# Performance work log

Hardware: AMD Instinct MI355X
Metric: run time of the kernel (lower is better)

The kernel has to match this reference:

```python
import jax, jax.numpy as jnp
import numpy as np

BOUND = np.array([[-4.0, 4.0], [-4.0, 4.0], [-2.0, 2.0]], dtype=np.float32)
N_PTS = 1048576
PLANE_C = 3
PLANE_RES = [128, 256, 512, 1024]
N_LEVELS = 16
F_PER = 2
T = 2 ** 16  # hashmap size (log2_hashmap_size=16)
BASE_RES = 16
FINEST = int(float((BOUND[:, 1] - BOUND[:, 0]).max()) / 0.02)  # 400
_growth = np.exp(np.log(FINEST / BASE_RES) / (N_LEVELS - 1))
HASH_RES = np.floor(BASE_RES * _growth ** np.arange(N_LEVELS)).astype(np.float32)
PRIMES = jnp.array([1, 2654435761, 805459861], dtype=jnp.uint32)


def setup_inputs() -> dict:
    key = jax.random.key(0)
    ks = jax.random.split(key, 32)
    lo = jnp.asarray(BOUND[:, 0]); hi = jnp.asarray(BOUND[:, 1])
    inp = {}
    inp['p'] = jax.random.uniform(ks[0], (N_PTS, 3), dtype=jnp.float32) * (hi - lo) + lo
    i = 1
    for li, r in enumerate(PLANE_RES):
        for name in ('xy', 'xz', 'yz'):
            inp[f'plane_{name}_{li}'] = 0.1 * jax.random.normal(ks[i], (PLANE_C, r, r), dtype=jnp.float32)
            i += 1
    inp['hash_table'] = jax.random.uniform(ks[i], (N_LEVELS, T, F_PER), dtype=jnp.float32, minval=-1e-4, maxval=1e-4); i += 1

    def lin(k, fi, fo):
        s = 1.0 / np.sqrt(fi)
        k1, k2 = jax.random.split(k)
        return (jax.random.uniform(k1, (fi, fo), minval=-s, maxval=s, dtype=jnp.float32),
                jax.random.uniform(k2, (fo,), minval=-s, maxval=s, dtype=jnp.float32))

    c_in = 12 * PLANE_C + N_LEVELS * F_PER  # 68
    inp['W0'], inp['b0'] = lin(ks[i], c_in, 64); i += 1
    inp['W1'], inp['b1'] = lin(ks[i], 64, 64); i += 1
    inp['Wo'], inp['bo'] = lin(ks[i], 64, 33); i += 1  # 1 sdf + 32 geo_feat
    inp['Wc0'], inp['bc0'] = lin(ks[i], 12 * PLANE_C + 32, 64); i += 1
    inp['Wc1'], inp['bc1'] = lin(ks[i], 64, 32); i += 1
    inp['Wco'], inp['bco'] = lin(ks[i], 32, 3); i += 1
    return inp


def sample_plane(plane, u, v):
    """Bilinear grid_sample, align_corners=True, padding_mode='border'.
    plane: (C,H,W); u indexes W, v indexes H; u,v in [-1,1]. Returns (N,C)."""
    C, H, W = plane.shape
    x = jnp.clip((u + 1.0) * 0.5 * (W - 1), 0.0, W - 1)
    y = jnp.clip((v + 1.0) * 0.5 * (H - 1), 0.0, H - 1)
    x0 = jnp.floor(x); y0 = jnp.floor(y)
    wx = x - x0; wy = y - y0
    x0i = x0.astype(jnp.int32); y0i = y0.astype(jnp.int32)
    x1i = jnp.minimum(x0i + 1, W - 1); y1i = jnp.minimum(y0i + 1, H - 1)
    g = lambda yi, xi: plane[:, yi, xi]  # (C,N)
    out = (g(y0i, x0i) * ((1 - wy) * (1 - wx)) + g(y0i, x1i) * ((1 - wy) * wx)
           + g(y1i, x0i) * (wy * (1 - wx)) + g(y1i, x1i) * (wy * wx))
    return out.T


def hash_encode(p01, table):
    """Multi-res hash grid (instant-ngp style). p01: (N,3) in [0,1]; table: (L,T,F) -> (N, L*F)."""
    res = jnp.asarray(HASH_RES)  # (L,)

    def level(r, tab):
        x = p01 * r
        x0 = jnp.floor(x)
        w = x - x0
        xi = x0.astype(jnp.uint32)  # (N,3)
        feat = jnp.zeros((p01.shape[0], F_PER), dtype=table.dtype)
        for dz in (0, 1):
            for dy in (0, 1):
                for dx in (0, 1):
                    c = xi + jnp.array([dx, dy, dz], dtype=jnp.uint32)
                    h = c * PRIMES[None, :]
                    idx = ((h[:, 0] ^ h[:, 1] ^ h[:, 2]) % T).astype(jnp.int32)
                    wgt = ((w[:, 0] if dx else 1 - w[:, 0])
                           * (w[:, 1] if dy else 1 - w[:, 1])
                           * (w[:, 2] if dz else 1 - w[:, 2]))
                    feat = feat + tab[idx] * wgt[:, None]
        return feat  # (N,F)

    feats = jax.vmap(level, in_axes=(0, 0))(res, table)  # (L,N,F)
    return jnp.transpose(feats, (1, 0, 2)).reshape(p01.shape[0], N_LEVELS * F_PER)


def _forward(p, plane_xy_0, plane_xz_0, plane_yz_0, plane_xy_1, plane_xz_1, plane_yz_1,
             plane_xy_2, plane_xz_2, plane_yz_2, plane_xy_3, plane_xz_3, plane_yz_3,
             hash_table, W0, b0, W1, b1, Wo, bo, Wc0, bc0, Wc1, bc1, Wco, bco):
    bound = jnp.asarray(BOUND)
    p_nor = (p - bound[:, 0]) / (bound[:, 1] - bound[:, 0]) * 2.0 - 1.0  # normalize_3d_coordinate
    u, v, w = p_nor[:, 0], p_nor[:, 1], p_nor[:, 2]
    levels = [(plane_xy_0, plane_xz_0, plane_yz_0), (plane_xy_1, plane_xz_1, plane_yz_1),
              (plane_xy_2, plane_xz_2, plane_yz_2), (plane_xy_3, plane_xz_3, plane_yz_3)]
    feats = []
    for pxy, pxz, pyz in levels:
        feats += [sample_plane(pxy, u, v), sample_plane(pxz, u, w), sample_plane(pyz, v, w)]
    plane_feat = jnp.concatenate(feats, axis=-1)  # (N, 36)
    hfeat = hash_encode((p_nor + 1.0) * 0.5, hash_table)  # (N, 32)
    # SDF branch
    h = jnp.concatenate([plane_feat, hfeat], axis=-1)  # (N, 68)
    h = jax.nn.relu(h @ W0 + b0)
    h = jax.nn.relu(h @ W1 + b1)
    sf = jnp.tanh(h @ Wo + bo)
    sdf, geo_feat = sf[:, :1], sf[:, 1:]
    # RGB branch
    c = jnp.concatenate([geo_feat, plane_feat], axis=-1)  # (N, 68)
    c = jax.nn.relu(c @ Wc0 + bc0)
    c = jax.nn.relu(c @ Wc1 + bc1)
    rgb = jax.nn.sigmoid(c @ Wco + bco)
    return jnp.concatenate([rgb, sdf], axis=-1)  # (N, 4)


def reference(p, plane_xy_0, plane_xz_0, plane_yz_0, plane_xy_1, plane_xz_1, plane_yz_1,
              plane_xy_2, plane_xz_2, plane_yz_2, plane_xy_3, plane_xz_3, plane_yz_3,
              hash_table, W0, b0, W1, b1, Wo, bo, Wc0, bc0, Wc1, bc1, Wco, bco):
    return _forward(p, plane_xy_0, plane_xz_0, plane_yz_0, plane_xy_1, plane_xz_1, plane_yz_1,
                    plane_xy_2, plane_xz_2, plane_yz_2, plane_xy_3, plane_xz_3, plane_yz_3,
                    hash_table, W0, b0, W1, b1, Wo, bo, Wc0, bc0, Wc1, bc1, Wco, bco)
```

## Files before the change

### kernel.cpp

```cpp
#include <hip/hip_runtime.h>

#define NPTS 1048576
#define NBKT 262144

typedef short bhalf8 __attribute__((ext_vector_type(8)));
typedef _Float16 halfv8 __attribute__((ext_vector_type(8)));
typedef float floatx4 __attribute__((ext_vector_type(4)));

#define WSZ 24320
#define FROWS 21
#define MLP_THREADS 1024
#define MLP_WAVES 16

#define PB_PLANES 16320
#define PB_HASH 4096
#define PB_HIST 4096

__device__ const float HRg[16] = {16.f, 19.f, 24.f, 30.f, 37.f, 46.f, 57.f, 71.f,
                                  89.f, 110.f, 136.f, 169.f, 210.f, 260.f, 322.f, 400.f};


__device__ __forceinline__ float my_tanh(float x) {
  float e = __expf(2.f * x);
  return 1.f - 2.f * __builtin_amdgcn_rcpf(e + 1.f);
}

__device__ __forceinline__ float my_sigmoid(float x) {
  return __builtin_amdgcn_rcpf(1.f + __expf(-x));
}

__device__ __forceinline__ unsigned short f2h(float v) {
  _Float16 h = (_Float16)v;
  unsigned short u;
  __builtin_memcpy(&u, &h, 2);
  return u;
}

__device__ __forceinline__ float h2f(unsigned short u) {
  _Float16 h;
  __builtin_memcpy(&h, &u, 2);
  return (float)h;
}

__device__ __forceinline__ float texch(uint2 t, int c) {
  unsigned short u = (c == 0) ? (unsigned short)(t.x & 0xffffu)
                   : (c == 1) ? (unsigned short)(t.x >> 16)
                              : (unsigned short)(t.y & 0xffffu);
  return h2f(u);
}

__device__ __forceinline__ unsigned mort6(unsigned x) {
  return (x & 1) | ((x & 2) << 2) | ((x & 4) << 4) |
         ((x & 8) << 6) | ((x & 16) << 8) | ((x & 32) << 10);
}

__device__ __forceinline__ unsigned morton_key(float px, float py, float pz) {
  float qx = (px + 4.f) * 0.125f, qy = (py + 4.f) * 0.125f, qz = (pz + 2.f) * 0.25f;
  unsigned kx = min(63, max(0, (int)(qx * 64.f)));
  unsigned ky = min(63, max(0, (int)(qy * 64.f)));
  unsigned kz = min(63, max(0, (int)(qz * 64.f)));
  return mort6(kx) | (mort6(ky) << 1) | (mort6(kz) << 2);
}

__device__ __forceinline__ unsigned hash_level(const unsigned* __restrict__ ht, int lv,
                                               float q0, float q1, float q2) {
  const float r = HRg[lv];
  float x0 = q0 * r, x1 = q1 * r, x2 = q2 * r;
  float f0 = floorf(x0), f1 = floorf(x1), f2 = floorf(x2);
  float w0 = x0 - f0, w1 = x1 - f1, w2 = x2 - f2;
  unsigned i0 = (unsigned)(int)f0, i1 = (unsigned)(int)f1, i2 = (unsigned)(int)f2;
  const unsigned* __restrict__ hb = ht + ((unsigned)lv << 16);
  unsigned tv[8];
#pragma unroll
  for (int dz = 0; dz < 2; ++dz)
#pragma unroll
    for (int dy = 0; dy < 2; ++dy)
#pragma unroll
      for (int dx = 0; dx < 2; ++dx) {
        unsigned h = (i0 + dx) ^ ((i1 + dy) * 2654435761u) ^ ((i2 + dz) * 805459861u);
        tv[dz * 4 + dy * 2 + dx] = hb[h & 65535u];
      }
  float a0 = 0.f, a1 = 0.f;
#pragma unroll
  for (int c = 0; c < 8; ++c) {
    const int dx = c & 1, dy = (c >> 1) & 1, dz = c >> 2;
    float wgt = (dx ? w0 : 1.f - w0) * (dy ? w1 : 1.f - w1) * (dz ? w2 : 1.f - w2);
    a0 = fmaf(h2f((unsigned short)(tv[c] & 0xffffu)), wgt, a0);
    a1 = fmaf(h2f((unsigned short)(tv[c] >> 16)), wgt, a1);
  }
  return (unsigned)f2h(a0) | ((unsigned)f2h(a1) << 16);
}


struct PrepParams {
  const float* psrc[12];
  ushort4* pdst[12];
  const float* hash;
  unsigned* hashb;
  const float* p;
  unsigned* hist;
};

__global__ __launch_bounds__(256) void prep_kernel(PrepParams P) {
  const int b = blockIdx.x;
  if (b < PB_PLANES) {
    const int CUM[13] = {0, 16384, 32768, 49152, 114688, 180224, 245760,
                         507904, 770048, 1032192, 2080768, 3129344, 4177920};
    const int RESL[12] = {128, 128, 128, 256, 256, 256, 512, 512, 512, 1024, 1024, 1024};
    const int s = b << 8;
    int pi = 0;
#pragma unroll
    for (int i = 1; i < 12; ++i)
      if (s >= CUM[i]) pi = i;
    const int li = s + threadIdx.x - CUM[pi];
    const int R = RESL[pi];
    const int n = R * R;
    const float* __restrict__ src = P.psrc[pi];
    ushort4 t;
    t.x = f2h(src[li]);
    t.y = f2h(src[n + li]);
    t.z = f2h(src[2 * n + li]);
    t.w = 0;
    P.pdst[pi][li] = t;
  } else if (b < PB_PLANES + PB_HASH) {
    const int i = ((b - PB_PLANES) << 8) + threadIdx.x;
    float2 v = *(const float2*)(P.hash + (size_t)i * 2);
    P.hashb[i] = (unsigned)f2h(v.x) | ((unsigned)f2h(v.y) << 16);
  } else {
    const int i = ((b - PB_PLANES - PB_HASH) << 8) + threadIdx.x;
    const float* pp = P.p + (size_t)i * 3;
    unsigned k = morton_key(pp[0], pp[1], pp[2]);
    atomicAdd(&P.hist[k], 1u);
  }
}


__global__ __launch_bounds__(256) void scan1_kernel(const unsigned* __restrict__ hist,
                                                    unsigned* __restrict__ partial) {
  __shared__ unsigned s[256];
  const int b = blockIdx.x, t = threadIdx.x;
  uint4 v = ((const uint4*)(hist + b * 1024))[t];
  s[t] = v.x + v.y + v.z + v.w;
  __syncthreads();
  for (int d = 128; d > 0; d >>= 1) {
    if (t < d) s[t] += s[t + d];
    __syncthreads();
  }
  if (t == 0) partial[b] = s[0];
}

__global__ __launch_bounds__(256) void scan2_kernel(const unsigned* __restrict__ partial,
                                                    unsigned* __restrict__ base) {
  __shared__ unsigned s[256];
  const int t = threadIdx.x;
  s[t] = partial[t];
  __syncthreads();
  for (int d = 1; d < 256; d <<= 1) {
    unsigned v = (t >= d) ? s[t - d] : 0u;
    __syncthreads();
    s[t] += v;
    __syncthreads();
  }
  base[t] = (t == 0) ? 0u : s[t - 1];
}

__global__ __launch_bounds__(256) void scan3_kernel(const unsigned* __restrict__ hist,
                                                    const unsigned* __restrict__ base,
                                                    unsigned* __restrict__ cursor) {
  __shared__ unsigned s[256];
  const int b = blockIdx.x, t = threadIdx.x;
  uint4 v = ((const uint4*)(hist + b * 1024))[t];
  unsigned sum = v.x + v.y + v.z + v.w;
  s[t] = sum;
  __syncthreads();
  for (int d = 1; d < 256; d <<= 1) {
    unsigned x = (t >= d) ? s[t - d] : 0u;
    __syncthreads();
    s[t] += x;
    __syncthreads();
  }
  unsigned off = base[b] + s[t] - sum;
  uint4 c;
  c.x = off;
  c.y = off + v.x;
  c.z = off + v.x + v.y;
  c.w = off + v.x + v.y + v.z;
  ((uint4*)(cursor + b * 1024))[t] = c;
}

__global__ __launch_bounds__(256) void scatter_kernel(const float* __restrict__ p,
                                                      unsigned* __restrict__ cursor,
                                                      unsigned* __restrict__ perm) {
  int i = blockIdx.x * 256 + threadIdx.x;
  const float* pp = p + (size_t)i * 3;
  unsigned k = morton_key(pp[0], pp[1], pp[2]);
  unsigned slot = atomicAdd(&cursor[k], 1u);
  perm[slot] = (unsigned)i;
}


__global__ __launch_bounds__(256) void repack_plane(const float* __restrict__ src,
                                                    ushort4* __restrict__ dst, int R) {
  int i = blockIdx.x * 256 + threadIdx.x;
  int n = R * R;
  if (i >= n) return;
  ushort4 t;
  t.x = f2h(src[i]);
  t.y = f2h(src[n + i]);
  t.z = f2h(src[2 * n + i]);
  t.w = 0;
  dst[i] = t;
}


__device__ __forceinline__ void sample3i(const uint2* __restrict__ pl,
                                         float a, float b, int R, float* f) {
  const float Rm1 = (float)(R - 1);
  float x = fminf(fmaxf((a + 1.f) * 0.5f * Rm1, 0.f), Rm1);
  float y = fminf(fmaxf((b + 1.f) * 0.5f * Rm1, 0.f), Rm1);
  float x0f = floorf(x), y0f = floorf(y);
  float wx = x - x0f, wy = y - y0f;
  int x0 = (int)x0f, y0 = (int)y0f;
  int x1 = min(x0 + 1, R - 1), y1 = min(y0 + 1, R - 1);
  float w00 = (1.f - wy) * (1.f - wx);
  float w01 = (1.f - wy) * wx;
  float w10 = wy * (1.f - wx);
  float w11 = wy * wx;
  uint2 t00 = pl[y0 * R + x0];
  uint2 t01 = pl[y0 * R + x1];
  uint2 t10 = pl[y1 * R + x0];
  uint2 t11 = pl[y1 * R + x1];
#pragma unroll
  for (int c = 0; c < 3; ++c) {
    f[c] = texch(t00, c) * w00 + texch(t01, c) * w01 +
           texch(t10, c) * w10 + texch(t11, c) * w11;
  }
}

__device__ __forceinline__ void sample3f(const float* __restrict__ pl,
                                         float a, float b, int R, float* f) {
  const float Rm1 = (float)(R - 1);
  float x = fminf(fmaxf((a + 1.f) * 0.5f * Rm1, 0.f), Rm1);
  float y = fminf(fmaxf((b + 1.f) * 0.5f * Rm1, 0.f), Rm1);
  float x0f = floorf(x), y0f = floorf(y);
  float wx = x - x0f, wy = y - y0f;
  int x0 = (int)x0f, y0 = (int)y0f;
  int x1 = min(x0 + 1, R - 1), y1 = min(y0 + 1, R - 1);
  float w00 = (1.f - wy) * (1.f - wx);
  float w01 = (1.f - wy) * wx;
  float w10 = wy * (1.f - wx);
  float w11 = wy * wx;
  int i00 = y0 * R + x0, i01 = y0 * R + x1;
  int i10 = y1 * R + x0, i11 = y1 * R + x1;
  const int R2 = R * R;
#pragma unroll
  for (int c = 0; c < 3; ++c) {
    const float* base = pl + c * R2;
    f[c] = base[i00] * w00 + base[i01] * w01 + base[i10] * w10 + base[i11] * w11;
  }
}


struct FeatParams {
  const float* p;
  const uint2* pli[12];
  const unsigned* perm;
  unsigned* fbuf;
};

template <bool SORT>
__global__ __launch_bounds__(256) void feat_kernel(FeatParams P) {
  int bid = blockIdx.x;
  if (SORT) bid = (bid & 7) * (NPTS / 256 / 8) + (bid >> 3);
  const int tid = bid * 256 + threadIdx.x;
  const int pid = SORT ? (int)P.perm[tid] : tid;

  const float* __restrict__ pp = P.p + (size_t)pid * 3;
  const float px = pp[0], py = pp[1], pz = pp[2];

  const float u = (px + 4.f) * 0.25f - 1.f;
  const float v = (py + 4.f) * 0.25f - 1.f;
  const float w = (pz + 2.f) * 0.5f - 1.f;

  float pf[36];
  {
    const int RES[4] = {128, 256, 512, 1024};
#pragma unroll
    for (int li = 0; li < 4; ++li) {
      sample3i(P.pli[li * 3 + 0], u, v, RES[li], &pf[li * 9 + 0]);
      sample3i(P.pli[li * 3 + 1], u, w, RES[li], &pf[li * 9 + 3]);
      sample3i(P.pli[li * 3 + 2], v, w, RES[li], &pf[li * 9 + 6]);
    }
  }
  unsigned* __restrict__ F = P.fbuf;
#pragma unroll
  for (int kk = 0; kk < 18; ++kk) {
    unsigned pk = (unsigned)f2h(pf[2 * kk]) | ((unsigned)f2h(pf[2 * kk + 1]) << 16);
    F[(size_t)kk * NPTS + tid] = pk;
  }
  F[(size_t)18 * NPTS + tid] = __float_as_uint((px + 4.f) * 0.125f);
  F[(size_t)19 * NPTS + tid] = __float_as_uint((py + 4.f) * 0.125f);
  F[(size_t)20 * NPTS + tid] = __float_as_uint((pz + 2.f) * 0.25f);
}


struct MlpWParams {
  const unsigned* fbuf;
  const unsigned* perm;
  const unsigned* hashb;
  const float* W0; const float* b0;
  const float* W1; const float* b1;
  const float* Wo; const float* bo;
  const float* Wc0; const float* bc0;
  const float* Wc1; const float* bc1;
  const float* Wco; const float* bco;
  float* out;
};

__device__ __forceinline__ void stage_w(const float* __restrict__ src, int K, int Nsrc,
                                        int STR, int NPAD, int OFF, short* Wlds, int tid) {
  const int total = NPAD * STR;
  for (int idx = tid; idx < total; idx += MLP_THREADS) {
    int c = idx / STR;
    int k = idx - c * STR;
    float val = (k < K && c < Nsrc) ? src[k * Nsrc + c] : 0.f;
    Wlds[OFF + idx] = (short)f2h(val);
  }
}

__device__ __forceinline__ void stage_b(const float* __restrict__ src, int Nsrc, int NPAD,
                                        int BOFF, float* Blds, int tid) {
  for (int j = tid; j < NPAD; j += MLP_THREADS) Blds[BOFF + j] = (j < Nsrc) ? src[j] : 0.f;
}

__device__ __forceinline__ halfv8 as_h8(bhalf8 s) {
  halfv8 h;
  __builtin_memcpy(&h, &s, 16);
  return h;
}

__device__ __forceinline__ halfv8 ldA(const unsigned* __restrict__ fbuf, int pt,
                                      int kkBase, int kkLim) {
  bhalf8 r;
#pragma unroll
  for (int j = 0; j < 4; ++j) {
    const int kk = kkBase + j;
    unsigned d = 0u;
    if (kk < kkLim) d = fbuf[(size_t)kk * NPTS + pt];
    r[2 * j] = (short)(d & 0xffffu);
    r[2 * j + 1] = (short)(d >> 16);
  }
  return as_h8(r);
}

__device__ __forceinline__ halfv8 frag4(unsigned d0, unsigned d1, unsigned d2, unsigned d3) {
  bhalf8 r;
  r[0] = (short)(d0 & 0xffffu); r[1] = (short)(d0 >> 16);
  r[2] = (short)(d1 & 0xffffu); r[3] = (short)(d1 >> 16);
  r[4] = (short)(d2 & 0xffffu); r[5] = (short)(d2 >> 16);
  r[6] = (short)(d3 & 0xffffu); r[7] = (short)(d3 >> 16);
  return as_h8(r);
}

__device__ __forceinline__ halfv8 ldS(const short* scr, int rowl, int grp, int s) {
  return *(const halfv8*)&scr[rowl * 72 + 32 * s + 8 * grp];
}

template <int NT, int KS, int OFF, int STR>
__device__ __forceinline__ void mlayer(const halfv8 (&af)[KS], floatx4 (&acc)[NT],
                                       const short* Wlds, int rowl, int grp) {
#pragma unroll
  for (int n = 0; n < NT; ++n) {
    floatx4 a{};
#pragma unroll
    for (int s = 0; s < KS; ++s) {
      const int wo = OFF + (16 * n + rowl) * STR + 32 * s + 8 * grp;
      const halfv8 bh = *(const halfv8*)&Wlds[wo];
      a = __builtin_amdgcn_mfma_f32_16x16x32_f16(af[s], bh, a, 0, 0, 0);
    }
    acc[n] = a;
  }
}

template <int NT>
__device__ __forceinline__ void relu_wr(const floatx4 (&acc)[NT], const float* Blds,
                                        int boff, short* scr, int rowl, int grp) {
#pragma unroll
  for (int n = 0; n < NT; ++n) {
    const float b = Blds[boff + 16 * n + rowl];
#pragma unroll
    for (int r = 0; r < 4; ++r) {
      float v = fmaxf(acc[n][r] + b, 0.f);
      scr[(grp * 4 + r) * 72 + 16 * n + rowl] = (short)f2h(v);
    }
  }
}

__device__ __forceinline__ void tanh_wr(const floatx4 (&acc)[3], const float* Blds,
                                        short* scr, float* ost, int rowl, int grp) {
#pragma unroll
  for (int n = 0; n < 3; ++n) {
    const float b = Blds[128 + 16 * n + rowl];
    const int c = 16 * n + rowl;
#pragma unroll
    for (int r = 0; r < 4; ++r) {
      float v = my_tanh(acc[n][r] + b);
      if (n == 0 && rowl == 0) ost[(grp * 4 + r) * 4 + 3] = v;
      if (c >= 1 && c <= 32) scr[(grp * 4 + r) * 72 + c - 1] = (short)f2h(v);
    }
  }
}

template <bool SORT>
__global__ __launch_bounds__(MLP_THREADS) void mlp_mfma(MlpWParams P) {
  __shared__ short Wlds[WSZ];
  __shared__ float Blds[288];
  __shared__ short Scr[MLP_WAVES * 16 * 72];
  __shared__ float Ost[MLP_WAVES][16][4];

  const int tid = threadIdx.x;

  stage_w(P.W0,  68, 64, 104, 64,     0, Wlds, tid);
  stage_w(P.W1,  64, 64,  72, 64,  6656, Wlds, tid);
  stage_w(P.Wo,  64, 33,  72, 48, 11264, Wlds, tid);
  stage_w(P.Wc0, 68, 64, 104, 64, 14720, Wlds, tid);
  stage_w(P.Wc1, 64, 32,  72, 32, 21376, Wlds, tid);
  stage_w(P.Wco, 32,  3,  40, 16, 23680, Wlds, tid);
  stage_b(P.b0,  64, 64,   0, Blds, tid);
  stage_b(P.b1,  64, 64,  64, Blds, tid);
  stage_b(P.bo,  33, 48, 128, Blds, tid);
  stage_b(P.bc0, 64, 64, 176, Blds, tid);
  stage_b(P.bc1, 32, 32, 240, Blds, tid);
  stage_b(P.bco,  3, 16, 272, Blds, tid);
  __syncthreads();

  const int wave = tid >> 6, lane = tid & 63;
  const int rowl = lane & 15, grp = lane >> 4;
  short* scr0 = &Scr[wave * 16 * 72];
  float* ost0 = &Ost[wave][0][0];

  const int lv0 = (grp == 0) ? 0 : (4 * grp - 2);

  for (int t = 0; t < 8; ++t) {
    const int wbase = ((blockIdx.x * 8 + t) * MLP_WAVES + wave) * 16;
    const int ptA = wbase + rowl;

    {
      const unsigned* __restrict__ F = P.fbuf;
      float qA0 = __uint_as_float(F[(size_t)18 * NPTS + ptA]);
      float qA1 = __uint_as_float(F[(size_t)19 * NPTS + ptA]);
      float qA2 = __uint_as_float(F[(size_t)20 * NPTS + ptA]);

      unsigned hA0, hA1, hA2, hA3;
      {
        const int l0 = lv0, l1 = lv0 + 1;
        const int l2 = (grp == 0) ? 14 : (lv0 + 2);
        const int l3 = (grp == 0) ? 15 : (lv0 + 3);
        hA0 = hash_level(P.hashb, l0, qA0, qA1, qA2);
        hA1 = hash_level(P.hashb, l1, qA0, qA1, qA2);
        hA2 = hash_level(P.hashb, l2, qA0, qA1, qA2);
        hA3 = hash_level(P.hashb, l3, qA0, qA1, qA2);
      }

      unsigned pA16 = F[(size_t)16 * NPTS + ptA], pA17 = F[(size_t)17 * NPTS + ptA];

      halfv8 s1A = (grp == 0) ? frag4(pA16, pA17, hA0, hA1) : frag4(hA0, hA1, hA2, hA3);
      halfv8 s2A = (grp == 0) ? frag4(hA2, hA3, 0u, 0u) : frag4(0u, 0u, 0u, 0u);

      halfv8 afA[3] = {ldA(P.fbuf, ptA, 4 * grp, 18), s1A, s2A};
      floatx4 accA[4];
      mlayer<4, 3, 0, 104>(afA, accA, Wlds, rowl, grp);
      relu_wr<4>(accA, Blds, 0, scr0, rowl, grp);
    }
    {
      halfv8 afA[2] = {ldS(scr0, rowl, grp, 0), ldS(scr0, rowl, grp, 1)};
      floatx4 accA[4];
      mlayer<4, 2, 6656, 72>(afA, accA, Wlds, rowl, grp);
      relu_wr<4>(accA, Blds, 64, scr0, rowl, grp);
    }
    {
      halfv8 afA[2] = {ldS(scr0, rowl, grp, 0), ldS(scr0, rowl, grp, 1)};
      floatx4 accA[3];
      mlayer<3, 2, 11264, 72>(afA, accA, Wlds, rowl, grp);
      tanh_wr(accA, Blds, scr0, ost0, rowl, grp);
    }
    {
      halfv8 afA[3] = {ldS(scr0, rowl, grp, 0),
                       ldA(P.fbuf, ptA, 0 + 4 * grp, 18),
                       ldA(P.fbuf, ptA, 16 + 4 * grp, 18)};
      floatx4 accA[4];
      mlayer<4, 3, 14720, 104>(afA, accA, Wlds, rowl, grp);
      relu_wr<4>(accA, Blds, 176, scr0, rowl, grp);
    }
    {
      halfv8 afA[2] = {ldS(scr0, rowl, grp, 0), ldS(scr0, rowl, grp, 1)};
      floatx4 accA[2];
      mlayer<2, 2, 21376, 72>(afA, accA, Wlds, rowl, grp);
      relu_wr<2>(accA, Blds, 240, scr0, rowl, grp);
    }
    {
      halfv8 afA[1] = {ldS(scr0, rowl, grp, 0)};
      floatx4 accA[1];
      mlayer<1, 1, 23680, 40>(afA, accA, Wlds, rowl, grp);
      const float b = Blds[272 + rowl];
#pragma unroll
      for (int r = 0; r < 4; ++r) {
        float vA = my_sigmoid(accA[0][r] + b);
        if (rowl < 3) ost0[(grp * 4 + r) * 4 + rowl] = vA;
      }
    }

    if (lane < 16) {
      float4 o = *(float4*)&Ost[wave][lane][0];
      int dst = SORT ? (int)P.perm[wbase + lane] : (wbase + lane);
      ((float4*)P.out)[dst] = o;
    }
  }
}


struct DecParams {
  const float* p;
  const float* pl[12];
  const uint2* pli[12];
  const float* hash;
  const float* W0; const float* b0;
  const float* W1; const float* b1;
  const float* Wo; const float* bo;
  const float* Wc0; const float* bc0;
  const float* Wc1; const float* bc1;
  const float* Wco; const float* bco;
  float* out;
};

template <bool ILV>
__global__ __launch_bounds__(256) void dec_kernel(DecParams P) {
  const int tid = blockIdx.x * 256 + threadIdx.x;

  const float* __restrict__ pp = P.p + (size_t)tid * 3;
  const float px = pp[0], py = pp[1], pz = pp[2];

  const float u = (px + 4.f) * 0.25f - 1.f;
  const float v = (py + 4.f) * 0.25f - 1.f;
  const float w = (pz + 2.f) * 0.5f - 1.f;

  float feat[68];
  {
    const int RES[4] = {128, 256, 512, 1024};
#pragma unroll
    for (int li = 0; li < 4; ++li) {
      if (ILV) {
        sample3i(P.pli[li * 3 + 0], u, v, RES[li], &feat[li * 9 + 0]);
        sample3i(P.pli[li * 3 + 1], u, w, RES[li], &feat[li * 9 + 3]);
        sample3i(P.pli[li * 3 + 2], v, w, RES[li], &feat[li * 9 + 6]);
      } else {
        sample3f(P.pl[li * 3 + 0], u, v, RES[li], &feat[li * 9 + 0]);
        sample3f(P.pl[li * 3 + 1], u, w, RES[li], &feat[li * 9 + 3]);
        sample3f(P.pl[li * 3 + 2], v, w, RES[li], &feat[li * 9 + 6]);
      }
    }
  }

  {
    const float q0 = (px + 4.f) * 0.125f;
    const float q1 = (py + 4.f) * 0.125f;
    const float q2 = (pz + 2.f) * 0.25f;
    const float* __restrict__ ht = P.hash;
#pragma unroll
    for (int l = 0; l < 16; ++l) {
      const float r = HRg[l];
      float x0 = q0 * r, x1 = q1 * r, x2 = q2 * r;
      float f0 = floorf(x0), f1 = floorf(x1), f2 = floorf(x2);
      float w0 = x0 - f0, w1 = x1 - f1, w2 = x2 - f2;
      unsigned i0 = (unsigned)(int)f0, i1 = (unsigned)(int)f1, i2 = (unsigned)(int)f2;
      float a0 = 0.f, a1 = 0.f;
#pragma unroll
      for (int dz = 0; dz < 2; ++dz)
#pragma unroll
        for (int dy = 0; dy < 2; ++dy)
#pragma unroll
          for (int dx = 0; dx < 2; ++dx) {
            unsigned h = (i0 + dx) ^ ((i1 + dy) * 2654435761u) ^ ((i2 + dz) * 805459861u);
            unsigned idx = h & 65535u;
            const float2 tv = *(const float2*)(ht + (((unsigned)l << 16) + idx) * 2);
            float wgt = (dx ? w0 : 1.f - w0) * (dy ? w1 : 1.f - w1) * (dz ? w2 : 1.f - w2);
            a0 = fmaf(tv.x, wgt, a0);
            a1 = fmaf(tv.y, wgt, a1);
          }
      feat[36 + l * 2] = a0;
      feat[36 + l * 2 + 1] = a1;
    }
  }

  float acc[64];
#pragma unroll
  for (int j = 0; j < 64; ++j) acc[j] = P.b0[j];
#pragma unroll
  for (int i = 0; i < 68; ++i) {
    const float a = feat[i];
    const float* wr = P.W0 + i * 64;
#pragma unroll
    for (int j = 0; j < 64; ++j) acc[j] = fmaf(a, wr[j], acc[j]);
  }
  float hid[64];
#pragma unroll
  for (int j = 0; j < 64; ++j) hid[j] = fmaxf(acc[j], 0.f);

#pragma unroll
  for (int j = 0; j < 64; ++j) acc[j] = P.b1[j];
#pragma unroll
  for (int i = 0; i < 64; ++i) {
    const float a = hid[i];
    const float* wr = P.W1 + i * 64;
#pragma unroll
    for (int j = 0; j < 64; ++j) acc[j] = fmaf(a, wr[j], acc[j]);
  }
#pragma unroll
  for (int j = 0; j < 64; ++j) hid[j] = fmaxf(acc[j], 0.f);

  float so[33];
#pragma unroll
  for (int j = 0; j < 33; ++j) so[j] = P.bo[j];
#pragma unroll
  for (int i = 0; i < 64; ++i) {
    const float a = hid[i];
    const float* wr = P.Wo + i * 33;
#pragma unroll
    for (int j = 0; j < 33; ++j) so[j] = fmaf(a, wr[j], so[j]);
  }
  const float sdf = my_tanh(so[0]);
  float geo[32];
#pragma unroll
  for (int j = 0; j < 32; ++j) geo[j] = my_tanh(so[j + 1]);

#pragma unroll
  for (int j = 0; j < 64; ++j) acc[j] = P.bc0[j];
#pragma unroll
  for (int i = 0; i < 32; ++i) {
    const float a = geo[i];
    const float* wr = P.Wc0 + i * 64;
#pragma unroll
    for (int j = 0; j < 64; ++j) acc[j] = fmaf(a, wr[j], acc[j]);
  }
#pragma unroll
  for (int i = 0; i < 36; ++i) {
    const float a = feat[i];
    const float* wr = P.Wc0 + (32 + i) * 64;
#pragma unroll
    for (int j = 0; j < 64; ++j) acc[j] = fmaf(a, wr[j], acc[j]);
  }
#pragma unroll
  for (int j = 0; j < 64; ++j) hid[j] = fmaxf(acc[j], 0.f);

  float c1[32];
#pragma unroll
  for (int j = 0; j < 32; ++j) c1[j] = P.bc1[j];
#pragma unroll
  for (int i = 0; i < 64; ++i) {
    const float a = hid[i];
    const float* wr = P.Wc1 + i * 32;
#pragma unroll
    for (int j = 0; j < 32; ++j) c1[j] = fmaf(a, wr[j], c1[j]);
  }

  float r0 = P.bco[0], r1 = P.bco[1], r2 = P.bco[2];
#pragma unroll
  for (int i = 0; i < 32; ++i) {
    const float a = fmaxf(c1[i], 0.f);
    r0 = fmaf(a, P.Wco[i * 3 + 0], r0);
    r1 = fmaf(a, P.Wco[i * 3 + 1], r1);
    r2 = fmaf(a, P.Wco[i * 3 + 2], r2);
  }

  float4 o;
  o.x = my_sigmoid(r0);
  o.y = my_sigmoid(r1);
  o.z = my_sigmoid(r2);
  o.w = sdf;
  ((float4*)P.out)[tid] = o;
}


extern "C" void kernel_launch(void* const* d_in, const int* in_sizes, int n_in,
                              void* d_out, int out_size, void* d_ws, size_t ws_size,
                              hipStream_t stream) {
  const int RES[4] = {128, 256, 512, 1024};
  const size_t planes_bytes = (size_t)3 * (128 * 128 + 256 * 256 + 512 * 512 + 1024 * 1024) * 8;
  const size_t hash_bytes = (size_t)16 * 65536 * 4;
  const size_t feat_bytes = (size_t)FROWS * NPTS * 4;
  const size_t perm_bytes = (size_t)NPTS * 4;
  const size_t hist_bytes = (size_t)NBKT * 4;
  const size_t need_full = planes_bytes + hash_bytes + feat_bytes + 64;
  const size_t need_sort = need_full + perm_bytes + 2 * hist_bytes + 4096;
  const size_t need_mid = planes_bytes + 64;

  char* wsp = (char*)d_ws;
  const float* p = (const float*)d_in[0];

  if (ws_size >= need_sort) {
    size_t off = 0;
    PrepParams PP;
    PP.p = p;
    PP.hash = (const float*)d_in[13];
    const uint2* pli[12];
    for (int i = 0; i < 12; ++i) {
      int R = RES[i / 3];
      PP.psrc[i] = (const float*)d_in[1 + i];
      PP.pdst[i] = (ushort4*)(wsp + off);
      pli[i] = (const uint2*)(wsp + off);
      off += (size_t)R * R * 8;
    }
    unsigned* hashb = (unsigned*)(wsp + off);
    PP.hashb = hashb;
    off += hash_bytes;
    unsigned* fbuf = (unsigned*)(wsp + off);
    off += feat_bytes;
    unsigned* perm = (unsigned*)(wsp + off);
    off += perm_bytes;
    unsigned* hist = (unsigned*)(wsp + off);
    off += hist_bytes;
    unsigned* cursor = (unsigned*)(wsp + off);
    off += hist_bytes;
    unsigned* partial = (unsigned*)(wsp + off);
    off += 1024;
    unsigned* base = (unsigned*)(wsp + off);
    off += 1024;
    PP.hist = hist;

    hipMemsetAsync(hist, 0, hist_bytes, stream);
    prep_kernel<<<PB_PLANES + PB_HASH + PB_HIST, 256, 0, stream>>>(PP);
    scan1_kernel<<<256, 256, 0, stream>>>(hist, partial);
    scan2_kernel<<<1, 256, 0, stream>>>(partial, base);
    scan3_kernel<<<256, 256, 0, stream>>>(hist, base, cursor);
    scatter_kernel<<<NPTS / 256, 256, 0, stream>>>(p, cursor, perm);

    FeatParams FP;
    FP.p = p;
    for (int i = 0; i < 12; ++i) FP.pli[i] = pli[i];
    FP.perm = perm;
    FP.fbuf = fbuf;
    feat_kernel<true><<<NPTS / 256, 256, 0, stream>>>(FP);

    MlpWParams MP;
    MP.fbuf = fbuf;
    MP.perm = perm;
    MP.hashb = hashb;
    MP.W0 = (const float*)d_in[14]; MP.b0 = (const float*)d_in[15];
    MP.W1 = (const float*)d_in[16]; MP.b1 = (const float*)d_in[17];
    MP.Wo = (const float*)d_in[18]; MP.bo = (const float*)d_in[19];
    MP.Wc0 = (const float*)d_in[20]; MP.bc0 = (const float*)d_in[21];
    MP.Wc1 = (const float*)d_in[22]; MP.bc1 = (const float*)d_in[23];
    MP.Wco = (const float*)d_in[24]; MP.bco = (const float*)d_in[25];
    MP.out = (float*)d_out;
    mlp_mfma<true><<<512, MLP_THREADS, 0, stream>>>(MP);
    return;
  }

  if (ws_size >= need_full) {
    size_t off = 0;
    PrepParams PP;
    PP.p = p;
    PP.hash = (const float*)d_in[13];
    const uint2* pli[12];
    for (int i = 0; i < 12; ++i) {
      int R = RES[i / 3];
      PP.psrc[i] = (const float*)d_in[1 + i];
      PP.pdst[i] = (ushort4*)(wsp + off);
      pli[i] = (const uint2*)(wsp + off);
      off += (size_t)R * R * 8;
    }
    unsigned* hashb = (unsigned*)(wsp + off);
    PP.hashb = hashb;
    off += hash_bytes;
    unsigned* fbuf = (unsigned*)(wsp + off);
    PP.hist = nullptr;

    prep_kernel<<<PB_PLANES + PB_HASH, 256, 0, stream>>>(PP);

    FeatParams FP;
    FP.p = p;
    for (int i = 0; i < 12; ++i) FP.pli[i] = pli[i];
    FP.perm = nullptr;
    FP.fbuf = fbuf;
    feat_kernel<false><<<NPTS / 256, 256, 0, stream>>>(FP);

    MlpWParams MP;
    MP.fbuf = fbuf;
    MP.perm = nullptr;
    MP.hashb = hashb;
    MP.W0 = (const float*)d_in[14]; MP.b0 = (const float*)d_in[15];
    MP.W1 = (const float*)d_in[16]; MP.b1 = (const float*)d_in[17];
    MP.Wo = (const float*)d_in[18]; MP.bo = (const float*)d_in[19];
    MP.Wc0 = (const float*)d_in[20]; MP.bc0 = (const float*)d_in[21];
    MP.Wc1 = (const float*)d_in[22]; MP.bc1 = (const float*)d_in[23];
    MP.Wco = (const float*)d_in[24]; MP.bco = (const float*)d_in[25];
    MP.out = (float*)d_out;
    mlp_mfma<false><<<512, MLP_THREADS, 0, stream>>>(MP);
    return;
  }

  DecParams P;
  P.p = p;
  for (int i = 0; i < 12; ++i) P.pl[i] = (const float*)d_in[1 + i];
  P.hash = (const float*)d_in[13];
  P.W0  = (const float*)d_in[14]; P.b0  = (const float*)d_in[15];
  P.W1  = (const float*)d_in[16]; P.b1  = (const float*)d_in[17];
  P.Wo  = (const float*)d_in[18]; P.bo  = (const float*)d_in[19];
  P.Wc0 = (const float*)d_in[20]; P.bc0 = (const float*)d_in[21];
  P.Wc1 = (const float*)d_in[22]; P.bc1 = (const float*)d_in[23];
  P.Wco = (const float*)d_in[24]; P.bco = (const float*)d_in[25];
  P.out = (float*)d_out;

  if (ws_size >= need_mid) {
    size_t off = 0;
    for (int i = 0; i < 12; ++i) {
      int R = RES[i / 3];
      int n = R * R;
      P.pli[i] = (const uint2*)(wsp + off);
      repack_plane<<<(n + 255) / 256, 256, 0, stream>>>(
          (const float*)d_in[1 + i], (ushort4*)(wsp + off), R);
      off += (size_t)n * 8;
    }
    dec_kernel<true><<<NPTS / 256, 256, 0, stream>>>(P);
  } else {
    for (int i = 0; i < 12; ++i) P.pli[i] = nullptr;
    dec_kernel<false><<<NPTS / 256, 256, 0, stream>>>(P);
  }
}
```

Measured before the change: 399.7 us.

## Swap MFMA operand order for vectorized epilogue stores, packed-half hash blend, reuse fragments

Swaps the A/B operands of the MFMA so each lane holds four consecutive output channels for one point. The ReLU epilogue can then write a packed short4 to LDS instead of four scattered halfword stores. The hash trilinear blend now uses packed half2 FMAs instead of float conversions. The plane-feature fragment and the p16/p17 words are kept in registers for the RGB layer instead of being reloaded from global memory. Accumulating the hash blend in half precision lowers accuracy, and the reused fragment depends on the feature column layout matching the second ldA.

New measurement: 388.8 us. -2.7%, faster.

```diff
diff --git a/kernel.cpp b/kernel.cpp
--- a/kernel.cpp
+++ b/kernel.cpp
@@ -5,6 +5,7 @@
 
 typedef short bhalf8 __attribute__((ext_vector_type(8)));
 typedef _Float16 halfv8 __attribute__((ext_vector_type(8)));
+typedef _Float16 halfv2 __attribute__((ext_vector_type(2)));
 typedef float floatx4 __attribute__((ext_vector_type(4)));
 
 #define WSZ 24320
@@ -80,15 +81,20 @@
         unsigned h = (i0 + dx) ^ ((i1 + dy) * 2654435761u) ^ ((i2 + dz) * 805459861u);
         tv[dz * 4 + dy * 2 + dx] = hb[h & 65535u];
       }
-  float a0 = 0.f, a1 = 0.f;
+  halfv2 acc2 = {(_Float16)0.f, (_Float16)0.f};
 #pragma unroll
   for (int c = 0; c < 8; ++c) {
     const int dx = c & 1, dy = (c >> 1) & 1, dz = c >> 2;
     float wgt = (dx ? w0 : 1.f - w0) * (dy ? w1 : 1.f - w1) * (dz ? w2 : 1.f - w2);
-    a0 = fmaf(h2f((unsigned short)(tv[c] & 0xffffu)), wgt, a0);
-    a1 = fmaf(h2f((unsigned short)(tv[c] >> 16)), wgt, a1);
-  }
-  return (unsigned)f2h(a0) | ((unsigned)f2h(a1) << 16);
+    halfv2 th;
+    __builtin_memcpy(&th, &tv[c], 4);
+    _Float16 wh = (_Float16)wgt;
+    halfv2 w2v = {wh, wh};
+    acc2 = th * w2v + acc2;
+  }
+  unsigned res;
+  __builtin_memcpy(&res, &acc2, 4);
+  return res;
 }
 
 
@@ -375,8 +381,8 @@
 #pragma unroll
     for (int s = 0; s < KS; ++s) {
       const int wo = OFF + (16 * n + rowl) * STR + 32 * s + 8 * grp;
-      const halfv8 bh = *(const halfv8*)&Wlds[wo];
-      a = __builtin_amdgcn_mfma_f32_16x16x32_f16(af[s], bh, a, 0, 0, 0);
+      const halfv8 wA = *(const halfv8*)&Wlds[wo];
+      a = __builtin_amdgcn_mfma_f32_16x16x32_f16(wA, af[s], a, 0, 0, 0);
     }
     acc[n] = a;
   }
@@ -387,12 +393,17 @@
                                         int boff, short* scr, int rowl, int grp) {
 #pragma unroll
   for (int n = 0; n < NT; ++n) {
-    const float b = Blds[boff + 16 * n + rowl];
-#pragma unroll
-    for (int r = 0; r < 4; ++r) {
-      float v = fmaxf(acc[n][r] + b, 0.f);
-      scr[(grp * 4 + r) * 72 + 16 * n + rowl] = (short)f2h(v);
-    }
+    const int cbase = 16 * n + 4 * grp;
+    short4 v4;
+    float v0 = fmaxf(acc[n][0] + Blds[boff + cbase + 0], 0.f);
+    float v1 = fmaxf(acc[n][1] + Blds[boff + cbase + 1], 0.f);
+    float v2 = fmaxf(acc[n][2] + Blds[boff + cbase + 2], 0.f);
+    float v3 = fmaxf(acc[n][3] + Blds[boff + cbase + 3], 0.f);
+    v4.x = (short)f2h(v0);
+    v4.y = (short)f2h(v1);
+    v4.z = (short)f2h(v2);
+    v4.w = (short)f2h(v3);
+    *(short4*)&scr[rowl * 72 + cbase] = v4;
   }
 }
 
@@ -400,13 +411,12 @@
                                         short* scr, float* ost, int rowl, int grp) {
 #pragma unroll
   for (int n = 0; n < 3; ++n) {
-    const float b = Blds[128 + 16 * n + rowl];
-    const int c = 16 * n + rowl;
 #pragma unroll
     for (int r = 0; r < 4; ++r) {
-      float v = my_tanh(acc[n][r] + b);
-      if (n == 0 && rowl == 0) ost[(grp * 4 + r) * 4 + 3] = v;
-      if (c >= 1 && c <= 32) scr[(grp * 4 + r) * 72 + c - 1] = (short)f2h(v);
+      const int c = 16 * n + 4 * grp + r;
+      float v = my_tanh(acc[n][r] + Blds[128 + c]);
+      if (c == 0) ost[rowl * 4 + 3] = v;
+      if (c >= 1 && c <= 32) scr[rowl * 72 + c - 1] = (short)f2h(v);
     }
   }
 }
@@ -445,6 +455,9 @@
     const int wbase = ((blockIdx.x * 8 + t) * MLP_WAVES + wave) * 16;
     const int ptA = wbase + rowl;
 
+    halfv8 af0A;
+    unsigned pA16, pA17;
+
     {
       const unsigned* __restrict__ F = P.fbuf;
       float qA0 = __uint_as_float(F[(size_t)18 * NPTS + ptA]);
@@ -462,12 +475,14 @@
         hA3 = hash_level(P.hashb, l3, qA0, qA1, qA2);
       }
 
-      unsigned pA16 = F[(size_t)16 * NPTS + ptA], pA17 = F[(size_t)17 * NPTS + ptA];
+      pA16 = F[(size_t)16 * NPTS + ptA];
+      pA17 = F[(size_t)17 * NPTS + ptA];
 
       halfv8 s1A = (grp == 0) ? frag4(pA16, pA17, hA0, hA1) : frag4(hA0, hA1, hA2, hA3);
       halfv8 s2A = (grp == 0) ? frag4(hA2, hA3, 0u, 0u) : frag4(0u, 0u, 0u, 0u);
 
-      halfv8 afA[3] = {ldA(P.fbuf, ptA, 4 * grp, 18), s1A, s2A};
+      af0A = ldA(P.fbuf, ptA, 4 * grp, 18);
+      halfv8 afA[3] = {af0A, s1A, s2A};
       floatx4 accA[4];
       mlayer<4, 3, 0, 104>(afA, accA, Wlds, rowl, grp);
       relu_wr<4>(accA, Blds, 0, scr0, rowl, grp);
@@ -485,9 +500,8 @@
       tanh_wr(accA, Blds, scr0, ost0, rowl, grp);
     }
     {
-      halfv8 afA[3] = {ldS(scr0, rowl, grp, 0),
-                       ldA(P.fbuf, ptA, 0 + 4 * grp, 18),
-                       ldA(P.fbuf, ptA, 16 + 4 * grp, 18)};
+      halfv8 s2 = (grp == 0) ? frag4(pA16, pA17, 0u, 0u) : frag4(0u, 0u, 0u, 0u);
+      halfv8 afA[3] = {ldS(scr0, rowl, grp, 0), af0A, s2};
       floatx4 accA[4];
       mlayer<4, 3, 14720, 104>(afA, accA, Wlds, rowl, grp);
       relu_wr<4>(accA, Blds, 176, scr0, rowl, grp);
@@ -502,11 +516,13 @@
       halfv8 afA[1] = {ldS(scr0, rowl, grp, 0)};
       floatx4 accA[1];
       mlayer<1, 1, 23680, 40>(afA, accA, Wlds, rowl, grp);
-      const float b = Blds[272 + rowl];
 #pragma unroll
       for (int r = 0; r < 4; ++r) {
-        float vA = my_sigmoid(accA[0][r] + b);
-        if (rowl < 3) ost0[(grp * 4 + r) * 4 + rowl] = vA;
+        const int c = 4 * grp + r;
+        if (c < 3) {
+          float vA = my_sigmoid(accA[0][r] + Blds[272 + c]);
+          ost0[rowl * 4 + c] = vA;
+        }
       }
     }
 
```
